# Kernel tuning notes

Hardware: AMD Instinct MI355X
Metric: run time of the kernel (lower is better)

Reference implementation:

```python
import jax, jax.numpy as jnp
import numpy as np

B, N, A, O, D, Q, H = 64, 4, 1024, 128, 256, 256, 128
NEG_INF = -1e30


def setup_inputs() -> dict:
    key = jax.random.key(0)
    ks = jax.random.split(key, 8)
    q = jax.random.normal(ks[0], (B, N, 1, Q), dtype=jnp.float32)
    att1 = jax.random.uniform(ks[1], (B, N, A, O), dtype=jnp.float32)
    obj_reps = jax.random.normal(ks[2], (B, O, D), dtype=jnp.float32)
    tags_attention = jax.random.randint(ks[3], (B, N, A), 0, 2, dtype=jnp.int32)
    W1 = jax.random.normal(ks[4], (D + Q, H), dtype=jnp.float32) / np.sqrt(D + Q)
    b1 = jnp.zeros((H,), dtype=jnp.float32)
    W2 = jax.random.normal(ks[5], (H, 1), dtype=jnp.float32) / np.sqrt(H)
    b2 = jnp.zeros((1,), dtype=jnp.float32)
    return {"q": q, "att1": att1, "obj_reps": obj_reps,
            "tags_attention": tags_attention,
            "W1": W1, "b1": b1, "W2": W2, "b2": b2, "t": 1}


def reference(q, att1, obj_reps, tags_attention, W1, b1, W2, b2, t):
    # v: [B,N,A,D] = att1 [B,N,A,O] @ obj_reps [B,O,D]
    v = jnp.einsum('bnao,bod->bnad', att1, obj_reps)
    # q broadcast over token dim A, concat -> [B,N,A,D+Q]
    q_proj = jnp.broadcast_to(q, v.shape[:3] + (q.shape[-1],))
    vq = jnp.concatenate([v, q_proj], axis=-1)
    # FCNet: Linear + ReLU (dropout is identity at inference)
    joint_repr = jax.nn.relu(vq @ W1 + b1)          # [B,N,A,H]
    logits = (joint_repr @ W2 + b2)[..., 0]          # [B,N,A]
    # temperature-scaled masked softmax over tokens
    masked = jnp.where(tags_attention > 0, logits / t, NEG_INF)
    att2 = jax.nn.softmax(masked, axis=-1)           # [B,N,A]
    # attention_last: [B,N,O] = att2 [B,N,1,A] @ att1 [B,N,A,O]
    return jnp.einsum('bna,bnao->bno', att2, att1)
```

## Files before the change

kernel.cpp:

```cpp
#include <hip/hip_runtime.h>
#include <math.h>

#define Bc 64
#define Nc 4
#define Ac 1024
#define Oc 128
#define Dc 256
#define Qc 256
#define Hc 128
#define BN (Bc*Nc)

using f4     = __attribute__((ext_vector_type(4))) float;
using f32x4  = __attribute__((ext_vector_type(4))) float;
using short8 = __attribute__((ext_vector_type(8))) short;
using us4    = __attribute__((ext_vector_type(4))) unsigned short;

__device__ inline float decode_t(const void* p) {
    int i = *(const int*)p;
    if (i >= 1 && i <= 1000000) return (float)i;
    return __int_as_float(i);
}

__device__ inline unsigned short bf16_rne(float x) {
    unsigned u = __builtin_bit_cast(unsigned, x);
    u += 0x7FFFu + ((u >> 16) & 1u);
    return (unsigned short)(u >> 16);
}

__device__ inline void split_bf16(float x, unsigned short& hi, unsigned short& lo) {
    unsigned u = __builtin_bit_cast(unsigned, x);
    hi = (unsigned short)(u >> 16);
    float hif = __builtin_bit_cast(float, u & 0xFFFF0000u);
    float lof = x - hif;
    lo = (unsigned short)(__builtin_bit_cast(unsigned, lof) >> 16);
}

__global__ __launch_bounds__(256) void prep_split_kernel(
    const float* __restrict__ obj, const float* __restrict__ W1,
    unsigned short* __restrict__ obj_hi, unsigned short* __restrict__ obj_lo,
    unsigned short* __restrict__ W1T_hi, unsigned short* __restrict__ W1T_lo)
{
    __shared__ float Ts[64][65];
    const int t = threadIdx.x;
    const int bid = blockIdx.x;

    if (bid < 1024) {
        size_t i0 = ((size_t)bid * 256 + t) * 8;
        f4 v0 = *(const f4*)(obj + i0);
        f4 v1 = *(const f4*)(obj + i0 + 4);
        short8 hi, lo;
        unsigned short h16, l16;
        #pragma unroll
        for (int j = 0; j < 4; j++) {
            split_bf16(v0[j], h16, l16); hi[j] = (short)h16; lo[j] = (short)l16;
        }
        #pragma unroll
        for (int j = 0; j < 4; j++) {
            split_bf16(v1[j], h16, l16); hi[4 + j] = (short)h16; lo[4 + j] = (short)l16;
        }
        *(short8*)(obj_hi + i0) = hi;
        *(short8*)(obj_lo + i0) = lo;
    } else {
        const int wb = bid - 1024;
        const int d0 = (wb & 3) * 64, h0 = (wb >> 2) * 64;
        const int r4 = t >> 6, c = t & 63;
        #pragma unroll
        for (int rr = 0; rr < 16; rr++) {
            int d = rr * 4 + r4;
            Ts[d][c] = W1[(size_t)(d0 + d) * Hc + h0 + c];
        }
        __syncthreads();
        #pragma unroll
        for (int rr = 0; rr < 16; rr++) {
            int hl = rr * 4 + r4;
            float v = Ts[c][hl];
            unsigned short h16, l16;
            split_bf16(v, h16, l16);
            W1T_hi[(size_t)(h0 + hl) * Dc + d0 + c] = h16;
            W1T_lo[(size_t)(h0 + hl) * Dc + d0 + c] = l16;
        }
    }
}

__global__ __launch_bounds__(256, 4) void prep_M2_kernel(
    const unsigned short* __restrict__ W1T_hi, const unsigned short* __restrict__ W1T_lo,
    const unsigned short* __restrict__ obj_hi, const unsigned short* __restrict__ obj_lo,
    unsigned short* __restrict__ Mt_hi, unsigned short* __restrict__ Mt_lo)
{
    const int t = threadIdx.x;
    const int wave = t >> 6, lane = t & 63;
    const int l15 = lane & 15, quad = lane >> 4;
    const int h0 = blockIdx.x * 64 + wave * 16;
    const int o0 = blockIdx.y * 32;
    const int b  = blockIdx.z;

    const size_t arow  = (size_t)(h0 + l15) * Dc;
    const size_t brow0 = ((size_t)b * Oc + o0 + l15) * Dc;
    const size_t brow1 = ((size_t)b * Oc + o0 + 16 + l15) * Dc;

    f32x4 acc0 = (f32x4)(0.f), acc1 = (f32x4)(0.f);
    #pragma unroll
    for (int ks = 0; ks < 8; ks++) {
        const int ko = ks * 32 + quad * 8;
        short8 Ah  = *(const short8*)(W1T_hi + arow + ko);
        short8 Al  = *(const short8*)(W1T_lo + arow + ko);
        short8 B0h = *(const short8*)(obj_hi + brow0 + ko);
        short8 B0l = *(const short8*)(obj_lo + brow0 + ko);
        short8 B1h = *(const short8*)(obj_hi + brow1 + ko);
        short8 B1l = *(const short8*)(obj_lo + brow1 + ko);
        acc0 = __builtin_amdgcn_mfma_f32_16x16x32_bf16(Al, B0l, acc0, 0, 0, 0);
        acc0 = __builtin_amdgcn_mfma_f32_16x16x32_bf16(Al, B0h, acc0, 0, 0, 0);
        acc0 = __builtin_amdgcn_mfma_f32_16x16x32_bf16(Ah, B0l, acc0, 0, 0, 0);
        acc0 = __builtin_amdgcn_mfma_f32_16x16x32_bf16(Ah, B0h, acc0, 0, 0, 0);
        acc1 = __builtin_amdgcn_mfma_f32_16x16x32_bf16(Al, B1l, acc1, 0, 0, 0);
        acc1 = __builtin_amdgcn_mfma_f32_16x16x32_bf16(Al, B1h, acc1, 0, 0, 0);
        acc1 = __builtin_amdgcn_mfma_f32_16x16x32_bf16(Ah, B1l, acc1, 0, 0, 0);
        acc1 = __builtin_amdgcn_mfma_f32_16x16x32_bf16(Ah, B1h, acc1, 0, 0, 0);
    }

    #pragma unroll
    for (int r = 0; r < 4; r++) {
        int hrow = h0 + quad * 4 + r;
        size_t base = ((size_t)b * Hc + hrow) * Oc + o0 + l15;
        unsigned short hh, ll;
        split_bf16(acc0[r], hh, ll);
        Mt_hi[base] = hh; Mt_lo[base] = ll;
        split_bf16(acc1[r], hh, ll);
        Mt_hi[base + 16] = hh; Mt_lo[base + 16] = ll;
    }
}

__global__ __launch_bounds__(512) void prep_qb_kernel(
    const float* __restrict__ q, const float* __restrict__ W1,
    const float* __restrict__ b1, float* __restrict__ qb)
{
    __shared__ float qs[256];
    __shared__ float red[4][128];
    const int t = threadIdx.x;
    const int bn = blockIdx.x;

    if (t < 256) qs[t] = q[bn * Qc + t];
    __syncthreads();

    const int h = t & 127, kq = t >> 7;
    float acc = 0.f;
    const float* w = W1 + (size_t)(Dc + kq * 64) * Hc + h;
    #pragma unroll 8
    for (int d = 0; d < 64; ++d)
        acc += qs[kq * 64 + d] * w[(size_t)d * Hc];
    red[kq][h] = acc;
    __syncthreads();

    if (t < 128)
        qb[bn * Hc + t] = b1[t] + red[0][t] + red[1][t] + red[2][t] + red[3][t];
}

__global__ __launch_bounds__(512, 4) void main_half_kernel(
    const float* __restrict__ att1, const int* __restrict__ tags,
    const unsigned short* __restrict__ Mt_hi, const unsigned short* __restrict__ Mt_lo,
    const float* __restrict__ qb, const float* __restrict__ W2,
    const float* __restrict__ b2, const void* __restrict__ tptr,
    float* __restrict__ out_part, float* __restrict__ z_part)
{
    __shared__ unsigned short A_s[64][136];
    __shared__ float A32_s[64][132];
    __shared__ float part2[64][9];
    __shared__ float part3[4][132];
    __shared__ float e_s[64];
    __shared__ float qb_s[128], w2_s[128];

    const int t    = threadIdx.x;
    const int lane = t & 63;
    const int wave = t >> 6;
    const int l15  = lane & 15;
    const int quad = lane >> 4;
    const int blk  = blockIdx.x;
    const int bn   = blk >> 1;
    const int half = blk & 1;
    const int b    = bn >> 2;
    const int hw   = wave * 16;

    const float* att_half = att1 + ((size_t)bn * Ac + half * 512) * Oc;

    f4 sv[4];
    #pragma unroll
    for (int s = 0; s < 4; s++) {
        int idx = t + 512 * s;
        sv[s] = *(const f4*)(att_half + (size_t)idx * 4);
    }

    const size_t brow = ((size_t)b * Hc + hw + l15) * Oc;
    short8 Bh[4], Bl[4];
    #pragma unroll
    for (int ks = 0; ks < 4; ks++) {
        const int ko = ks * 32 + quad * 8;
        Bh[ks] = *(const short8*)(Mt_hi + brow + ko);
        Bl[ks] = *(const short8*)(Mt_lo + brow + ko);
    }

    if (t < 128) { qb_s[t] = qb[bn * Hc + t]; w2_s[t] = W2[t]; }
    int tg_cur = (t < 64) ? tags[(size_t)bn * Ac + half * 512 + t] : 0;
    const float b2v  = b2[0];
    const float tval = decode_t(tptr);

    float z_reg = 0.f, out_reg = 0.f;

    for (int tile = 0; tile < 8; ++tile) {
        if (tile > 0 && t < 128) {
            float s = 0.f;
            #pragma unroll
            for (int g = 0; g < 4; g++) s += part3[g][t];
            out_reg += s;
        }
        #pragma unroll
        for (int s = 0; s < 4; s++) {
            int idx = t + 512 * s;
            int r = idx >> 5, c4 = idx & 31;
            us4 h4;
            #pragma unroll
            for (int j = 0; j < 4; j++) h4[j] = bf16_rne(sv[s][j]);
            *(us4*)&A_s[r][c4 * 4] = h4;
            *(f4*)&A32_s[r][c4 * 4] = sv[s];
        }
        __syncthreads();

        int tg_next = 0;
        if (tile < 7) {
            const float* np = att_half + (size_t)(tile + 1) * 64 * Oc;
            #pragma unroll
            for (int s = 0; s < 4; s++) {
                int idx = t + 512 * s;
                sv[s] = *(const f4*)(np + (size_t)idx * 4);
            }
            if (t < 64) tg_next = tags[(size_t)bn * Ac + half * 512 + (tile + 1) * 64 + t];
        }

        f32x4 acc[4];
        #pragma unroll
        for (int i = 0; i < 4; i++) acc[i] = (f32x4)(0.f);
        #pragma unroll
        for (int ks = 0; ks < 4; ks++) {
            const int ko = ks * 32 + quad * 8;
            #pragma unroll
            for (int i = 0; i < 4; i++) {
                short8 ah = *(const short8*)&A_s[i * 16 + l15][ko];
                acc[i] = __builtin_amdgcn_mfma_f32_16x16x32_bf16(ah, Bh[ks], acc[i], 0, 0, 0);
                acc[i] = __builtin_amdgcn_mfma_f32_16x16x32_bf16(ah, Bl[ks], acc[i], 0, 0, 0);
            }
        }

        {
            const float qbv = qb_s[hw + l15], w2v = w2_s[hw + l15];
            float p[4][4];
            #pragma unroll
            for (int i = 0; i < 4; i++)
                #pragma unroll
                for (int r = 0; r < 4; r++) {
                    float v = acc[i][r] + qbv;
                    v = v > 0.f ? v : 0.f;
                    p[i][r] = v * w2v;
                }
            #pragma unroll
            for (int m = 1; m <= 8; m <<= 1)
                #pragma unroll
                for (int i = 0; i < 4; i++)
                    #pragma unroll
                    for (int r = 0; r < 4; r++)
                        p[i][r] += __shfl_xor(p[i][r], m);
            if (l15 == 0) {
                #pragma unroll
                for (int i = 0; i < 4; i++)
                    #pragma unroll
                    for (int r = 0; r < 4; r++)
                        part2[i * 16 + quad * 4 + r][wave] = p[i][r];
            }
        }
        __syncthreads();

        if (t < 64) {
            float sum = b2v;
            #pragma unroll
            for (int x = 0; x < 8; x++) sum += part2[t][x];
            float logit = sum / tval;
            float e = (tg_cur > 0) ? __expf(logit) : 0.f;
            e_s[t] = e;
            z_reg += e;
        }
        __syncthreads();

        {
            const int o = t & 127;
            const int g = t >> 7;
            float accum = 0.f;
            #pragma unroll
            for (int a = 0; a < 16; a++)
                accum += e_s[g * 16 + a] * A32_s[g * 16 + a][o];
            part3[g][o] = accum;
        }
        __syncthreads();
        tg_cur = tg_next;
    }

    if (t < 128) {
        float s = 0.f;
        #pragma unroll
        for (int g = 0; g < 4; g++) s += part3[g][t];
        out_reg += s;
        out_part[(size_t)blk * 128 + t] = out_reg;
    }
    if (t < 64) {
        float z = z_reg;
        #pragma unroll
        for (int off = 32; off > 0; off >>= 1) z += __shfl_down(z, off);
        if (t == 0) z_part[blk] = z;
    }
}

__global__ __launch_bounds__(128) void finalize_kernel(
    const float* __restrict__ out_part, const float* __restrict__ z_part,
    float* __restrict__ out)
{
    const int bn = blockIdx.x;
    const int t  = threadIdx.x;
    const float Z = z_part[bn * 2] + z_part[bn * 2 + 1];
    const float v = out_part[(size_t)(bn * 2) * 128 + t]
                  + out_part[(size_t)(bn * 2 + 1) * 128 + t];
    out[(size_t)bn * 128 + t] = v / Z;
}

extern "C" void kernel_launch(void* const* d_in, const int* in_sizes, int n_in,
                              void* d_out, int out_size, void* d_ws, size_t ws_size,
                              hipStream_t stream)
{
    (void)in_sizes; (void)n_in; (void)out_size; (void)ws_size;

    const float* q    = (const float*)d_in[0];
    const float* att1 = (const float*)d_in[1];
    const float* obj  = (const float*)d_in[2];
    const int*   tags = (const int*)d_in[3];
    const float* W1   = (const float*)d_in[4];
    const float* b1   = (const float*)d_in[5];
    const float* W2   = (const float*)d_in[6];
    const float* b2   = (const float*)d_in[7];
    const void*  tptr = (const void*)d_in[8];
    float* out = (float*)d_out;

    char* wsb = (char*)d_ws;
    unsigned short* Mt_hi  = (unsigned short*)wsb;
    unsigned short* Mt_lo  = (unsigned short*)(wsb + (size_t) 2*1024*1024);
    float* qbuf            = (float*)         (wsb + (size_t) 4*1024*1024);
    float* out_part        = (float*)         (wsb + (size_t) 5*1024*1024);
    float* z_part          = (float*)         (wsb + (size_t) 6*1024*1024);
    unsigned short* W1T_hi = (unsigned short*)(wsb + (size_t) 7*1024*1024);
    unsigned short* W1T_lo = (unsigned short*)(wsb + (size_t) 7*1024*1024 + 64*1024);
    unsigned short* obj_hi = (unsigned short*)(wsb + (size_t) 8*1024*1024);
    unsigned short* obj_lo = (unsigned short*)(wsb + (size_t)12*1024*1024);

    prep_split_kernel<<<dim3(1032), 256, 0, stream>>>(obj, W1, obj_hi, obj_lo,
                                                      W1T_hi, W1T_lo);
    prep_M2_kernel<<<dim3(2, 4, Bc), 256, 0, stream>>>(W1T_hi, W1T_lo, obj_hi, obj_lo,
                                                       Mt_hi, Mt_lo);
    prep_qb_kernel<<<dim3(BN), 512, 0, stream>>>(q, W1, b1, qbuf);
    main_half_kernel<<<dim3(2 * BN), 512, 0, stream>>>(att1, tags, Mt_hi, Mt_lo,
                                                       qbuf, W2, b2, tptr,
                                                       out_part, z_part);
    finalize_kernel<<<dim3(BN), 128, 0, stream>>>(out_part, z_part, out);
}
```

Measured before the change: 245.7 us.

## Use DPP row reductions and keep per-thread output accumulators across tiles

Replaces the shuffle-based 16-lane reduction of logit partials with DPP row-rotate adds. Each partial is reduced and stored to shared memory right away, so the 4x4 partial array no longer has to stay live. The weighted att1 accumulation now has each thread hold a 4-wide output vector in registers across all tiles, read with vectorized LDS loads. The per-tile cross-group reduction through part3 is deferred to a single reduction over 16 groups at the end, which removes per-tile LDS traffic and the serial work done by only 128 threads.

```diff
diff --git a/kernel.cpp b/kernel.cpp
--- a/kernel.cpp
+++ b/kernel.cpp
@@ -33,6 +33,20 @@
     float hif = __builtin_bit_cast(float, u & 0xFFFF0000u);
     float lof = x - hif;
     lo = (unsigned short)(__builtin_bit_cast(unsigned, lof) >> 16);
+}
+
+template<int CTRL>
+__device__ inline float dpp_ror_add(float x) {
+    int yi = __builtin_amdgcn_update_dpp(0, __builtin_bit_cast(int, x),
+                                         CTRL, 0xf, 0xf, true);
+    return x + __builtin_bit_cast(float, yi);
+}
+__device__ inline float row16_sum(float v) {
+    v = dpp_ror_add<0x128>(v);
+    v = dpp_ror_add<0x124>(v);
+    v = dpp_ror_add<0x122>(v);
+    v = dpp_ror_add<0x121>(v);
+    return v;
 }
 
 __global__ __launch_bounds__(256) void prep_split_kernel(
@@ -165,7 +179,7 @@
     __shared__ unsigned short A_s[64][136];
     __shared__ float A32_s[64][132];
     __shared__ float part2[64][9];
-    __shared__ float part3[4][132];
+    __shared__ float part3[16][132];
     __shared__ float e_s[64];
     __shared__ float qb_s[128], w2_s[128];
 
@@ -179,6 +193,8 @@
     const int half = blk & 1;
     const int b    = bn >> 2;
     const int hw   = wave * 16;
+    const int g3   = t >> 5;
+    const int o4   = (t & 31) * 4;
 
     const float* att_half = att1 + ((size_t)bn * Ac + half * 512) * Oc;
 
@@ -203,15 +219,10 @@
     const float b2v  = b2[0];
     const float tval = decode_t(tptr);
 
-    float z_reg = 0.f, out_reg = 0.f;
+    float z_reg = 0.f;
+    f4 out4 = {0.f, 0.f, 0.f, 0.f};
 
     for (int tile = 0; tile < 8; ++tile) {
-        if (tile > 0 && t < 128) {
-            float s = 0.f;
-            #pragma unroll
-            for (int g = 0; g < 4; g++) s += part3[g][t];
-            out_reg += s;
-        }
         #pragma unroll
         for (int s = 0; s < 4; s++) {
             int idx = t + 512 * s;
@@ -251,29 +262,16 @@
 
         {
             const float qbv = qb_s[hw + l15], w2v = w2_s[hw + l15];
-            float p[4][4];
             #pragma unroll
             for (int i = 0; i < 4; i++)
                 #pragma unroll
                 for (int r = 0; r < 4; r++) {
                     float v = acc[i][r] + qbv;
                     v = v > 0.f ? v : 0.f;
-                    p[i][r] = v * w2v;
+                    float s = row16_sum(v * w2v);
+                    if (l15 == 0)
+                        part2[i * 16 + quad * 4 + r][wave] = s;
                 }
-            #pragma unroll
-            for (int m = 1; m <= 8; m <<= 1)
-                #pragma unroll
-                for (int i = 0; i < 4; i++)
-                    #pragma unroll
-                    for (int r = 0; r < 4; r++)
-                        p[i][r] += __shfl_xor(p[i][r], m);
-            if (l15 == 0) {
-                #pragma unroll
-                for (int i = 0; i < 4; i++)
-                    #pragma unroll
-                    for (int r = 0; r < 4; r++)
-                        part2[i * 16 + quad * 4 + r][wave] = p[i][r];
-            }
         }
         __syncthreads();
 
@@ -288,25 +286,27 @@
         }
         __syncthreads();
 
-        {
-            const int o = t & 127;
-            const int g = t >> 7;
-            float accum = 0.f;
-            #pragma unroll
-            for (int a = 0; a < 16; a++)
-                accum += e_s[g * 16 + a] * A32_s[g * 16 + a][o];
-            part3[g][o] = accum;
+        #pragma unroll
+        for (int a = 0; a < 4; a++) {
+            const int row = g3 * 4 + a;
+            const float ev = e_s[row];
+            f4 v = *(const f4*)&A32_s[row][o4];
+            out4[0] += ev * v[0];
+            out4[1] += ev * v[1];
+            out4[2] += ev * v[2];
+            out4[3] += ev * v[3];
         }
         __syncthreads();
         tg_cur = tg_next;
     }
 
+    *(f4*)&part3[g3][o4] = out4;
+    __syncthreads();
     if (t < 128) {
         float s = 0.f;
         #pragma unroll
-        for (int g = 0; g < 4; g++) s += part3[g][t];
-        out_reg += s;
-        out_part[(size_t)blk * 128 + t] = out_reg;
+        for (int g = 0; g < 16; g++) s += part3[g][t];
+        out_part[(size_t)blk * 128 + t] = s;
     }
     if (t < 64) {
         float z = z_reg;
```

Result: faster. 240.8 us (-2.0%).
